# Kernel tuning notes

Hardware: AMD Instinct MI355X
Metric: run time of the kernel (lower is better)

Reference implementation:

```python
import jax, jax.numpy as jnp
import numpy as np

B, T, D, H = 2, 2048, 1024, 16
HD = D // H

def setup_inputs() -> dict:
    key = jax.random.key(0)
    ks = jax.random.split(key, 6)
    x = jax.random.normal(ks[0], (B, T, D), dtype=jnp.float32)
    periods = jax.random.randint(ks[1], (B, H), 0, 16, dtype=jnp.int64)
    w_qkv = jax.random.normal(ks[2], (D, 3 * D), dtype=jnp.float32) * 0.02
    b_qkv = jnp.zeros((3 * D,), dtype=jnp.float32)
    w_out = jax.random.normal(ks[3], (D, D), dtype=jnp.float32) * 0.02
    b_out = jnp.zeros((D,), dtype=jnp.float32)
    return {"x": x, "periods": periods, "w_qkv": w_qkv, "b_qkv": b_qkv,
            "w_out": w_out, "b_out": b_out}

def reference(x, periods, w_qkv, b_qkv, w_out, b_out):
    b, t, d = x.shape
    h = periods.shape[1]
    hd = d // h
    qkv = x @ w_qkv + b_qkv                     # (B,T,3D)
    qkv = qkv.reshape(b, t, 3, h, hd).transpose(2, 0, 3, 1, 4)
    q, k, v = qkv[0], qkv[1], qkv[2]            # each (B,H,T,hd)
    # periodic + causal mask, fully vectorized over (B,H)
    p = jnp.maximum(periods, 1).astype(jnp.int32)[:, :, None, None]  # (B,H,1,1)
    i = jnp.arange(t, dtype=jnp.int32)[:, None]
    j = jnp.arange(t, dtype=jnp.int32)[None, :]
    causal = (j <= i)[None, None]                                    # (1,1,T,T)
    periodic = jnp.mod((i - j)[None, None], p) == 0                  # (B,H,T,T)
    valid = causal & periodic
    scores = jnp.einsum('bhqd,bhkd->bhqk', q, k) / jnp.sqrt(jnp.float32(hd))
    scores = jnp.where(valid, scores, -jnp.inf)  # diagonal always valid -> no NaN rows
    attn = jax.nn.softmax(scores, axis=-1)
    out = jnp.einsum('bhqk,bhkd->bhqd', attn, v)
    out = out.transpose(0, 2, 1, 3).reshape(b, t, d)
    return out @ w_out + b_out
```

## Files before the change

kernel.cpp:

```cpp
#include <hip/hip_runtime.h>
#include <math.h>

#define B_  2
#define T_  2048
#define D_  1024
#define H_  16
#define HD_ 64
#define VTS (T_ + 64)

typedef float    f32x4  __attribute__((ext_vector_type(4)));
typedef _Float16 half8  __attribute__((ext_vector_type(8)));
typedef _Float16 half4v __attribute__((ext_vector_type(4)));

#define GLOAD_LDS16(g, l)                                                     \
    __builtin_amdgcn_global_load_lds(                                         \
        (__attribute__((address_space(1))) void*)(g),                         \
        (__attribute__((address_space(3))) void*)(l), 16, 0, 0)

__device__ __forceinline__ void transpose_tile(
    const float* __restrict__ in, _Float16* __restrict__ out,
    int R, int C, int r0, int c0, int tid)
{
    __shared__ float tile[32][33];
    const int tx = tid & 31, ty = tid >> 5;
    #pragma unroll
    for (int q = 0; q < 4; ++q)
        tile[ty + 8 * q][tx] = in[(size_t)(r0 + ty + 8 * q) * C + c0 + tx];
    __syncthreads();
    #pragma unroll
    for (int q = 0; q < 4; ++q)
        out[(size_t)(c0 + ty + 8 * q) * R + r0 + tx] = (_Float16)tile[tx][ty + 8 * q];
}

__global__ __launch_bounds__(256) void prep_kernel(
    const float* __restrict__ x, _Float16* __restrict__ x16,
    const float* __restrict__ w_qkv, _Float16* __restrict__ wqkvT,
    const float* __restrict__ w_out, _Float16* __restrict__ woutT)
{
    const int bx = blockIdx.x, tid = threadIdx.x;
    if (bx < 4096) {
        const int i = (bx * 256 + tid) * 4;
        float4 v = *(const float4*)(x + i);
        half4v h;
        h[0] = (_Float16)v.x; h[1] = (_Float16)v.y;
        h[2] = (_Float16)v.z; h[3] = (_Float16)v.w;
        *(half4v*)(x16 + i) = h;
    } else if (bx < 7168) {
        const int bi = bx - 4096;
        transpose_tile(w_qkv, wqkvT, D_, 3 * D_,
                       (bi / 96) * 32, (bi % 96) * 32, tid);
    } else {
        const int bi = bx - 7168;
        transpose_tile(w_out, woutT, D_, D_,
                       (bi / 32) * 32, (bi % 32) * 32, tid);
    }
}

#define GEMM_BODY()                                                           \
    __shared__ __align__(16) _Float16 As[128 * 64];                           \
    __shared__ __align__(16) _Float16 Bs[128 * 64];                           \
    const int tid  = threadIdx.x;                                             \
    const int lane = tid & 63;                                                \
    const int w    = tid >> 6;                                                \
    const int wm   = (w >> 1) * 64;                                           \
    const int wn   = (w & 1) * 64;                                            \
    const int srow = lane >> 3;                                     \
    const int sseg = (lane & 7) ^ srow;               \
    const _Float16* gA = A  + (size_t)(blockIdx.y * 128 + w * 32 + srow) * K + sseg * 8; \
    const _Float16* gB = Bt + (size_t)(blockIdx.x * 128 + w * 32 + srow) * K + sseg * 8; \
    _Float16* lA = &As[(w * 32) * 64];                                        \
    _Float16* lB = &Bs[(w * 32) * 64];                                        \
    f32x4 acc[4][4];                                                          \
    _Pragma("unroll")                                                         \
    for (int i = 0; i < 4; ++i)                                               \
        _Pragma("unroll")                                                     \
        for (int j = 0; j < 4; ++j)                                           \
            _Pragma("unroll")                                                 \
            for (int rr = 0; rr < 4; ++rr) acc[i][j][rr] = 0.f;               \
    const int fr  = lane & 15;                                                \
    const int fq  = lane >> 4;                                                \
    const int fsw = fr & 7;                                                   \
    for (int k0 = 0; k0 < K; k0 += 64) {                                      \
        _Pragma("unroll")                                                     \
        for (int i = 0; i < 4; ++i) {                                         \
            GLOAD_LDS16(gA + (size_t)(i * 8) * K + k0, lA + i * 8 * 64);      \
            GLOAD_LDS16(gB + (size_t)(i * 8) * K + k0, lB + i * 8 * 64);      \
        }                                                                     \
        __syncthreads();                                                      \
        _Pragma("unroll")                                                     \
        for (int kk = 0; kk < 2; ++kk) {                                      \
            half8 af[4], bf[4];                                               \
            _Pragma("unroll")                                                 \
            for (int i = 0; i < 4; ++i)                                       \
                af[i] = *(const half8*)&As[(wm + i * 16 + fr) * 64 +          \
                                           ((kk * 4 + fq) ^ fsw) * 8];        \
            _Pragma("unroll")                                                 \
            for (int j = 0; j < 4; ++j)                                       \
                bf[j] = *(const half8*)&Bs[(wn + j * 16 + fr) * 64 +          \
                                           ((kk * 4 + fq) ^ fsw) * 8];        \
            _Pragma("unroll")                                                 \
            for (int i = 0; i < 4; ++i)                                       \
                _Pragma("unroll")                                             \
                for (int j = 0; j < 4; ++j)                                   \
                    acc[i][j] = __builtin_amdgcn_mfma_f32_16x16x32_f16(       \
                        af[i], bf[j], acc[i][j], 0, 0, 0);                    \
        }                                                                     \
        __syncthreads();                                                      \
    }

template <typename OutT>
__global__ __launch_bounds__(256, 4) void gemm_bt_f16(
    const _Float16* __restrict__ A, const _Float16* __restrict__ Bt,
    const float* __restrict__ bias, OutT* __restrict__ C,
    int M, int N, int K)
{
    GEMM_BODY()
    #pragma unroll
    for (int j = 0; j < 4; ++j) {
        const int col = blockIdx.x * 128 + wn + j * 16 + fr;
        const float bv = bias[col];
        #pragma unroll
        for (int i = 0; i < 4; ++i) {
            const int row = blockIdx.y * 128 + wm + i * 16 + fq * 4;
            #pragma unroll
            for (int rr = 0; rr < 4; ++rr)
                C[(size_t)(row + rr) * N + col] = (OutT)(acc[i][j][rr] + bv);
        }
    }
}

__global__ __launch_bounds__(256, 4) void gemm_bt_f16_qkv(
    const _Float16* __restrict__ A, const _Float16* __restrict__ Bt,
    const float* __restrict__ bias, _Float16* __restrict__ C,
    int M, int N, int K)
{
    GEMM_BODY()
    #pragma unroll
    for (int j = 0; j < 4; ++j) {
        const int col = blockIdx.x * 128 + wn + j * 16 + fr;
        const float bv = bias[col];
        const int which = col >> 10;
        const int hh    = (col >> 6) & 15;
        const int e     = col & 63;
        #pragma unroll
        for (int i = 0; i < 4; ++i) {
            const int row = blockIdx.y * 128 + wm + i * 16 + fq * 4;
            #pragma unroll
            for (int rr = 0; rr < 4; ++rr) {
                const int rowr = row + rr;
                const int b2 = rowr >> 11, t = rowr & 2047;
                const size_t dst =
                    (((size_t)(b2 * 16 + hh) * 3 + which) * 2048 + t) * 64 + e;
                C[dst] = (_Float16)(acc[i][j][rr] + bv);
            }
        }
    }
}

__global__ __launch_bounds__(256) void vt_gather_kernel(
    const _Float16* __restrict__ qkv, const int* __restrict__ periods,
    _Float16* __restrict__ vt)
{
    __shared__ _Float16 tile[64][72];
    const int bh = blockIdx.y;
    int p = periods[bh]; if (p < 1) p = 1;
    const int c0 = blockIdx.x * 64;
    const int tid = threadIdx.x;
    const int rr = tid >> 2, seg = (tid & 3) * 16;

    const int c = c0 + rr;
    int r = 0, off = 0;
    for (; r < p - 1; ++r) {
        const int n = (T_ - 1 - r) / p + 1;
        if (c < off + n) break;
        off += n;
    }
    const int t = r + (c - off) * p;

    const size_t hs = (size_t)T_ * HD_;
    const _Float16* vrow = qkv + ((size_t)bh * 3 + 2) * hs + (size_t)t * HD_ + seg;
    *(half8*)&tile[rr][seg]     = *(const half8*)(vrow);
    *(half8*)&tile[rr][seg + 8] = *(const half8*)(vrow + 8);
    __syncthreads();

    _Float16* dst = vt + ((size_t)bh * HD_ + rr) * VTS + c0 + seg;
    half8 o0, o1;
    #pragma unroll
    for (int i = 0; i < 8; ++i) o0[i] = tile[seg + i][rr];
    #pragma unroll
    for (int i = 0; i < 8; ++i) o1[i] = tile[seg + 8 + i][rr];
    *(half8*)(dst)     = o0;
    *(half8*)(dst + 8) = o1;
}

__global__ __launch_bounds__(256, 4) void attn_mfma7_kernel(
    const _Float16* __restrict__ qkv, const _Float16* __restrict__ vt,
    const int* __restrict__ periods, _Float16* __restrict__ ao)
{
    __shared__ __align__(16) _Float16 Kt0[64 * 64], Kt1[64 * 64];
    __shared__ __align__(16) _Float16 Vt0[64 * 64], Vt1[64 * 64];
    __shared__ __align__(16) _Float16 Ps[4][16 * 64];

    const int bh = blockIdx.x;
    int p = periods[bh]; if (p < 1) p = 1;

    int tix = blockIdx.y;
    int r = -1, q0 = 0, n_r = 0, off = 0;
    for (int rr2 = 0; rr2 < p; ++rr2) {
        const int n  = (T_ - 1 - rr2) / p + 1;
        const int nt = (n + 63) >> 6;
        if (tix < nt) { r = rr2; n_r = n; q0 = (nt - 1 - tix) << 6; break; }
        tix -= nt;
        off += n;
    }
    if (r < 0) return;
    const int qn  = min(64, n_r - q0);
    const int kts = (q0 + qn + 63) >> 6;

    const int tid = threadIdx.x, lane = tid & 63, w = tid >> 6;
    const int ln = lane & 15, fq = lane >> 4;
    const int lsw = ln & 7;

    const size_t hs = (size_t)T_ * HD_;
    const _Float16* qb  = qkv + (size_t)(bh * 3) * hs;
    const _Float16* kb  = qb + hs;
    const _Float16* vtb = vt + (size_t)bh * HD_ * VTS + off;

    const int Lrow = lane >> 3;
    const int Lseg = (lane & 7) ^ Lrow;

    half8 aq0, aq1;
    {
        const int qi = min(q0 + w * 16 + ln, n_r - 1);
        const _Float16* qrow = qb + (size_t)(r + qi * p) * HD_;
        aq0 = *(const half8*)(qrow + fq * 8);
        aq1 = *(const half8*)(qrow + 32 + fq * 8);
    }

    f32x4 Od[4];
    float lp[4];
    #pragma unroll
    for (int nt = 0; nt < 4; ++nt)
        #pragma unroll
        for (int rr = 0; rr < 4; ++rr) Od[nt][rr] = 0.f;
    #pragma unroll
    for (int rr = 0; rr < 4; ++rr) lp[rr] = 0.f;

#define STAGE_KV(ktn, KT, VT) do {                                            \
        const int k0n = (ktn) << 6;                                           \
        _Pragma("unroll")                                                     \
        for (int i = 0; i < 2; ++i) {                                         \
            const int rowl = w * 16 + i * 8 + Lrow;                           \
            const int kj   = min(k0n + rowl, n_r - 1);                        \
            GLOAD_LDS16(kb + (size_t)(r + kj * p) * HD_ + Lseg * 8,           \
                        &KT[(w * 16 + i * 8) * 64]);                          \
            GLOAD_LDS16(vtb + (size_t)rowl * VTS + k0n + Lseg * 8,            \
                        &VT[(w * 16 + i * 8) * 64]);                          \
        }                                                                     \
    } while (0)

#define ATTN_ITER(kt, KT, VT, KTN, VTN) do {                                  \
        const int k0 = (kt) << 6;                                             \
        if ((kt) + 1 < kts) STAGE_KV((kt) + 1, KTN, VTN);                     \
        half8 bk0[4], bk1[4];                                                 \
        _Pragma("unroll")                                                     \
        for (int nt = 0; nt < 4; ++nt) {                                      \
            const int row = nt * 16 + ln;                                     \
            bk0[nt] = *(const half8*)&KT[row * 64 + ((fq ^ lsw) << 3)];       \
            bk1[nt] = *(const half8*)&KT[row * 64 + (((4 + fq) ^ lsw) << 3)]; \
        }                                                                     \
        f32x4 Sd[4];                                                          \
        _Pragma("unroll")                                                     \
        for (int nt = 0; nt < 4; ++nt) {                                      \
            _Pragma("unroll")                                                 \
            for (int rr = 0; rr < 4; ++rr) Sd[nt][rr] = 0.f;                  \
            Sd[nt] = __builtin_amdgcn_mfma_f32_16x16x32_f16(aq0, bk0[nt], Sd[nt], 0, 0, 0); \
            Sd[nt] = __builtin_amdgcn_mfma_f32_16x16x32_f16(aq1, bk1[nt], Sd[nt], 0, 0, 0); \
        }                                                                     \
        const bool diag = (k0 + 64 > q0);                                     \
        _Pragma("unroll")                                                     \
        for (int rr = 0; rr < 4; ++rr) {                                      \
            const int q_abs = q0 + w * 16 + fq * 4 + rr;                      \
            float s0 = Sd[0][rr] * 0.125f, s1 = Sd[1][rr] * 0.125f;           \
            float s2 = Sd[2][rr] * 0.125f, s3 = Sd[3][rr] * 0.125f;           \
            if (diag) {                                                       \
                if (k0 +  0 + ln > q_abs) s0 = -INFINITY;                     \
                if (k0 + 16 + ln > q_abs) s1 = -INFINITY;                     \
                if (k0 + 32 + ln > q_abs) s2 = -INFINITY;                     \
                if (k0 + 48 + ln > q_abs) s3 = -INFINITY;                     \
            }                                                                 \
            const float e0 = __expf(s0), e1 = __expf(s1);                     \
            const float e2 = __expf(s2), e3 = __expf(s3);                     \
            lp[rr] += (e0 + e1) + (e2 + e3);                                  \
            const int prow = fq * 4 + rr, rsw = prow & 7;                     \
            _Float16* pb = &Ps[w][prow * 64] + (ln & 7);                      \
            pb[(((ln >> 3) + 0) ^ rsw) << 3] = (_Float16)e0;                  \
            pb[(((ln >> 3) + 2) ^ rsw) << 3] = (_Float16)e1;                  \
            pb[(((ln >> 3) + 4) ^ rsw) << 3] = (_Float16)e2;                  \
            pb[(((ln >> 3) + 6) ^ rsw) << 3] = (_Float16)e3;                  \
        }                                                                     \
        half8 ap0 = *(const half8*)&Ps[w][ln * 64 + ((fq ^ lsw) << 3)];       \
        half8 ap1 = *(const half8*)&Ps[w][ln * 64 + (((4 + fq) ^ lsw) << 3)]; \
        _Pragma("unroll")                                                     \
        for (int nt = 0; nt < 4; ++nt) {                                      \
            const int row = nt * 16 + ln;                                     \
            half8 bv0 = *(const half8*)&VT[row * 64 + ((fq ^ lsw) << 3)];     \
            half8 bv1 = *(const half8*)&VT[row * 64 + (((4 + fq) ^ lsw) << 3)]; \
            Od[nt] = __builtin_amdgcn_mfma_f32_16x16x32_f16(ap0, bv0, Od[nt], 0, 0, 0); \
            Od[nt] = __builtin_amdgcn_mfma_f32_16x16x32_f16(ap1, bv1, Od[nt], 0, 0, 0); \
        }                                                                     \
        __syncthreads();                                                      \
    } while (0)

    STAGE_KV(0, Kt0, Vt0);
    __syncthreads();

    for (int kt = 0; kt < kts; kt += 2) {
        ATTN_ITER(kt, Kt0, Vt0, Kt1, Vt1);
        if (kt + 1 < kts)
            ATTN_ITER(kt + 1, Kt1, Vt1, Kt0, Vt0);
    }

    const int bb = bh >> 4, hh = bh & 15;
    #pragma unroll
    for (int rr = 0; rr < 4; ++rr) {
        float l = lp[rr];
        l += __shfl_xor(l, 1);
        l += __shfl_xor(l, 2);
        l += __shfl_xor(l, 4);
        l += __shfl_xor(l, 8);
        const int qq = w * 16 + fq * 4 + rr;
        if (q0 + qq < n_r) {
            const int t = r + (q0 + qq) * p;
            const float inv = 1.f / l;
            _Float16* orow = ao + ((size_t)bb * T_ + t) * D_ + hh * HD_;
            #pragma unroll
            for (int nt = 0; nt < 4; ++nt)
                orow[nt * 16 + ln] = (_Float16)(Od[nt][rr] * inv);
        }
    }
#undef STAGE_KV
#undef ATTN_ITER
}

extern "C" void kernel_launch(void* const* d_in, const int* in_sizes, int n_in,
                              void* d_out, int out_size, void* d_ws, size_t ws_size,
                              hipStream_t stream)
{
    const float* x       = (const float*)d_in[0];
    const int*   periods = (const int*)  d_in[1];
    const float* w_qkv   = (const float*)d_in[2];
    const float* b_qkv   = (const float*)d_in[3];
    const float* w_out   = (const float*)d_in[4];
    const float* b_out   = (const float*)d_in[5];
    float*       out     = (float*)d_out;

    const int M = B_ * T_;

    _Float16* x16   = (_Float16*)d_ws;
    _Float16* wqkvT = x16   + (size_t)M * D_;
    _Float16* qkv16 = wqkvT + (size_t)(3 * D_) * D_;
    _Float16* ao16  = qkv16 + (size_t)M * 3 * D_;
    _Float16* woutT = ao16  + (size_t)M * D_;
    _Float16* vt16  = woutT + (size_t)D_ * D_;

    prep_kernel<<<8192, 256, 0, stream>>>(x, x16, w_qkv, wqkvT, w_out, woutT);

    gemm_bt_f16_qkv<<<dim3((3 * D_) / 128, M / 128), 256, 0, stream>>>(
        x16, wqkvT, b_qkv, qkv16, M, 3 * D_, D_);

    vt_gather_kernel<<<dim3(T_ / 64, B_ * H_), 256, 0, stream>>>(
        qkv16, periods, vt16);

    attn_mfma7_kernel<<<dim3(B_ * H_, 48), 256, 0, stream>>>(
        qkv16, vt16, periods, ao16);

    gemm_bt_f16<float><<<dim3(D_ / 128, M / 128), 256, 0, stream>>>(
        ao16, woutT, b_out, out, M, D_, D_);
}
```

Before: 183.0 us.

## Remap block IDs for XCD locality, add 128x64 out GEMM, set MFMA priority

```diff
diff --git a/kernel.cpp b/kernel.cpp
--- a/kernel.cpp
+++ b/kernel.cpp
@@ -56,7 +56,7 @@
     }
 }
 
-#define GEMM_BODY()                                                           \
+#define GEMM_BODY(BX, BY)                                                     \
     __shared__ __align__(16) _Float16 As[128 * 64];                           \
     __shared__ __align__(16) _Float16 Bs[128 * 64];                           \
     const int tid  = threadIdx.x;                                             \
@@ -66,8 +66,8 @@
     const int wn   = (w & 1) * 64;                                            \
     const int srow = lane >> 3;                                     \
     const int sseg = (lane & 7) ^ srow;               \
-    const _Float16* gA = A  + (size_t)(blockIdx.y * 128 + w * 32 + srow) * K + sseg * 8; \
-    const _Float16* gB = Bt + (size_t)(blockIdx.x * 128 + w * 32 + srow) * K + sseg * 8; \
+    const _Float16* gA = A  + (size_t)((BY) * 128 + w * 32 + srow) * K + sseg * 8; \
+    const _Float16* gB = Bt + (size_t)((BX) * 128 + w * 32 + srow) * K + sseg * 8; \
     _Float16* lA = &As[(w * 32) * 64];                                        \
     _Float16* lB = &Bs[(w * 32) * 64];                                        \
     f32x4 acc[4][4];                                                          \
@@ -108,43 +108,26 @@
         __syncthreads();                                                      \
     }
 
-template <typename OutT>
-__global__ __launch_bounds__(256, 4) void gemm_bt_f16(
-    const _Float16* __restrict__ A, const _Float16* __restrict__ Bt,
-    const float* __restrict__ bias, OutT* __restrict__ C,
-    int M, int N, int K)
-{
-    GEMM_BODY()
-    #pragma unroll
-    for (int j = 0; j < 4; ++j) {
-        const int col = blockIdx.x * 128 + wn + j * 16 + fr;
-        const float bv = bias[col];
-        #pragma unroll
-        for (int i = 0; i < 4; ++i) {
-            const int row = blockIdx.y * 128 + wm + i * 16 + fq * 4;
-            #pragma unroll
-            for (int rr = 0; rr < 4; ++rr)
-                C[(size_t)(row + rr) * N + col] = (OutT)(acc[i][j][rr] + bv);
-        }
-    }
-}
-
 __global__ __launch_bounds__(256, 4) void gemm_bt_f16_qkv(
     const _Float16* __restrict__ A, const _Float16* __restrict__ Bt,
     const float* __restrict__ bias, _Float16* __restrict__ C,
     int M, int N, int K)
 {
-    GEMM_BODY()
+    const int fid  = blockIdx.x;
+    const int wgid = (fid & 7) * 96 + (fid >> 3);
+    const int bx   = wgid % 24;
+    const int by   = wgid / 24;
+    GEMM_BODY(bx, by)
     #pragma unroll
     for (int j = 0; j < 4; ++j) {
-        const int col = blockIdx.x * 128 + wn + j * 16 + fr;
+        const int col = bx * 128 + wn + j * 16 + fr;
         const float bv = bias[col];
         const int which = col >> 10;
         const int hh    = (col >> 6) & 15;
         const int e     = col & 63;
         #pragma unroll
         for (int i = 0; i < 4; ++i) {
-            const int row = blockIdx.y * 128 + wm + i * 16 + fq * 4;
+            const int row = by * 128 + wm + i * 16 + fq * 4;
             #pragma unroll
             for (int rr = 0; rr < 4; ++rr) {
                 const int rowr = row + rr;
@@ -157,14 +140,88 @@
     }
 }
 
+__global__ __launch_bounds__(256, 4) void gemm_out_128x64(
+    const _Float16* __restrict__ A, const _Float16* __restrict__ Bt,
+    const float* __restrict__ bias, float* __restrict__ C,
+    int M, int N, int K)
+{
+    __shared__ __align__(16) _Float16 As[128 * 64];
+    __shared__ __align__(16) _Float16 Bs[64 * 64];
+    const int fid  = blockIdx.x;
+    const int wgid = (fid & 7) * 64 + (fid >> 3);
+    const int bx   = wgid & 15;
+    const int by   = wgid >> 4;
+    const int tid  = threadIdx.x;
+    const int lane = tid & 63;
+    const int w    = tid >> 6;
+    const int srow = lane >> 3;
+    const int sseg = (lane & 7) ^ srow;
+    const _Float16* gA = A  + (size_t)(by * 128 + w * 32 + srow) * K + sseg * 8;
+    const _Float16* gB = Bt + (size_t)(bx * 64  + w * 16 + srow) * K + sseg * 8;
+    _Float16* lA = &As[(w * 32) * 64];
+    _Float16* lB = &Bs[(w * 16) * 64];
+    f32x4 acc[2][4];
+    #pragma unroll
+    for (int i = 0; i < 2; ++i)
+        #pragma unroll
+        for (int j = 0; j < 4; ++j)
+            #pragma unroll
+            for (int rr = 0; rr < 4; ++rr) acc[i][j][rr] = 0.f;
+    const int fr  = lane & 15;
+    const int fq  = lane >> 4;
+    const int fsw = fr & 7;
+    for (int k0 = 0; k0 < K; k0 += 64) {
+        #pragma unroll
+        for (int i = 0; i < 4; ++i)
+            GLOAD_LDS16(gA + (size_t)(i * 8) * K + k0, lA + i * 8 * 64);
+        #pragma unroll
+        for (int i = 0; i < 2; ++i)
+            GLOAD_LDS16(gB + (size_t)(i * 8) * K + k0, lB + i * 8 * 64);
+        __syncthreads();
+        #pragma unroll
+        for (int kk = 0; kk < 2; ++kk) {
+            half8 af[2], bf[4];
+            #pragma unroll
+            for (int i = 0; i < 2; ++i)
+                af[i] = *(const half8*)&As[(w * 32 + i * 16 + fr) * 64 +
+                                           ((kk * 4 + fq) ^ fsw) * 8];
+            #pragma unroll
+            for (int j = 0; j < 4; ++j)
+                bf[j] = *(const half8*)&Bs[(j * 16 + fr) * 64 +
+                                           ((kk * 4 + fq) ^ fsw) * 8];
+            #pragma unroll
+            for (int i = 0; i < 2; ++i)
+                #pragma unroll
+                for (int j = 0; j < 4; ++j)
+                    acc[i][j] = __builtin_amdgcn_mfma_f32_16x16x32_f16(
+                        af[i], bf[j], acc[i][j], 0, 0, 0);
+        }
+        __syncthreads();
+    }
+    #pragma unroll
+    for (int j = 0; j < 4; ++j) {
+        const int col = bx * 64 + j * 16 + fr;
+        const float bv = bias[col];
+        #pragma unroll
+        for (int i = 0; i < 2; ++i) {
+            const int row = by * 128 + w * 32 + i * 16 + fq * 4;
+            #pragma unroll
+            for (int rr = 0; rr < 4; ++rr)
+                C[(size_t)(row + rr) * N + col] = acc[i][j][rr] + bv;
+        }
+    }
+}
+
 __global__ __launch_bounds__(256) void vt_gather_kernel(
     const _Float16* __restrict__ qkv, const int* __restrict__ periods,
     _Float16* __restrict__ vt)
 {
     __shared__ _Float16 tile[64][72];
-    const int bh = blockIdx.y;
+    const int fid = blockIdx.x;
+    const int s   = fid >> 3;
+    const int bh  = (fid & 7) + 8 * (s >> 5);
+    const int c0  = (s & 31) * 64;
     int p = periods[bh]; if (p < 1) p = 1;
-    const int c0 = blockIdx.x * 64;
     const int tid = threadIdx.x;
     const int rr = tid >> 2, seg = (tid & 3) * 16;
 
@@ -201,10 +258,13 @@
     __shared__ __align__(16) _Float16 Vt0[64 * 64], Vt1[64 * 64];
     __shared__ __align__(16) _Float16 Ps[4][16 * 64];
 
-    const int bh = blockIdx.x;
+    const int fid = blockIdx.x;
+    const int s   = fid >> 3;
+    const int bh  = (fid & 7) + 8 * (s / 48);
+    int tix = s % 48;
+
     int p = periods[bh]; if (p < 1) p = 1;
 
-    int tix = blockIdx.y;
     int r = -1, q0 = 0, n_r = 0, off = 0;
     for (int rr2 = 0; rr2 < p; ++rr2) {
         const int n  = (T_ - 1 - rr2) / p + 1;
@@ -270,6 +330,7 @@
             bk1[nt] = *(const half8*)&KT[row * 64 + (((4 + fq) ^ lsw) << 3)]; \
         }                                                                     \
         f32x4 Sd[4];                                                          \
+        __builtin_amdgcn_s_setprio(1);                                        \
         _Pragma("unroll")                                                     \
         for (int nt = 0; nt < 4; ++nt) {                                      \
             _Pragma("unroll")                                                 \
@@ -277,6 +338,7 @@
             Sd[nt] = __builtin_amdgcn_mfma_f32_16x16x32_f16(aq0, bk0[nt], Sd[nt], 0, 0, 0); \
             Sd[nt] = __builtin_amdgcn_mfma_f32_16x16x32_f16(aq1, bk1[nt], Sd[nt], 0, 0, 0); \
         }                                                                     \
+        __builtin_amdgcn_s_setprio(0);                                        \
         const bool diag = (k0 + 64 > q0);                                     \
         _Pragma("unroll")                                                     \
         for (int rr = 0; rr < 4; ++rr) {                                      \
@@ -301,6 +363,7 @@
         }                                                                     \
         half8 ap0 = *(const half8*)&Ps[w][ln * 64 + ((fq ^ lsw) << 3)];       \
         half8 ap1 = *(const half8*)&Ps[w][ln * 64 + (((4 + fq) ^ lsw) << 3)]; \
+        __builtin_amdgcn_s_setprio(1);                                        \
         _Pragma("unroll")                                                     \
         for (int nt = 0; nt < 4; ++nt) {                                      \
             const int row = nt * 16 + ln;                                     \
@@ -309,6 +372,7 @@
             Od[nt] = __builtin_amdgcn_mfma_f32_16x16x32_f16(ap0, bv0, Od[nt], 0, 0, 0); \
             Od[nt] = __builtin_amdgcn_mfma_f32_16x16x32_f16(ap1, bv1, Od[nt], 0, 0, 0); \
         }                                                                     \
+        __builtin_amdgcn_s_setprio(0);                                        \
         __syncthreads();                                                      \
     } while (0)
 
@@ -366,15 +430,13 @@
 
     prep_kernel<<<8192, 256, 0, stream>>>(x, x16, w_qkv, wqkvT, w_out, woutT);
 
-    gemm_bt_f16_qkv<<<dim3((3 * D_) / 128, M / 128), 256, 0, stream>>>(
+    gemm_bt_f16_qkv<<<768, 256, 0, stream>>>(
         x16, wqkvT, b_qkv, qkv16, M, 3 * D_, D_);
 
-    vt_gather_kernel<<<dim3(T_ / 64, B_ * H_), 256, 0, stream>>>(
-        qkv16, periods, vt16);
-
-    attn_mfma7_kernel<<<dim3(B_ * H_, 48), 256, 0, stream>>>(
-        qkv16, vt16, periods, ao16);
-
-    gemm_bt_f16<float><<<dim3(D_ / 128, M / 128), 256, 0, stream>>>(
+    vt_gather_kernel<<<1024, 256, 0, stream>>>(qkv16, periods, vt16);
+
+    attn_mfma7_kernel<<<1536, 256, 0, stream>>>(qkv16, vt16, periods, ao16);
+
+    gemm_out_128x64<<<512, 256, 0, stream>>>(
         ao16, woutT, b_out, out, M, D_, D_);
 }
```

Result: faster. 171.5 us (-6.3%).
